# Kernel optimization log

Hardware: AMD Instinct MI355X
Metric: run time of the kernel (lower is better)

## Reference

```python
import jax, jax.numpy as jnp
import numpy as np

C = 64          # channels
HEADS = 4       # num_heads -> head_dim = 16
HID = int(C * 2.66)  # 170, GDFN hidden channels
B, H, W = 2, 256, 256


def conv1x1(x, w):
    # x: (b,c,h,w), w: (o,c) -> pointwise conv, no bias
    return jnp.einsum('bchw,oc->bohw', x, w)


def dwconv3x3(x, w):
    # depthwise 3x3, SAME padding; w: (C,1,3,3)
    return jax.lax.conv_general_dilated(
        x, w, window_strides=(1, 1), padding='SAME',
        feature_group_count=x.shape[1],
        dimension_numbers=('NCHW', 'OIHW', 'NCHW'))


def layer_norm_c(x, w, b):
    # torch: LayerNorm over channel dim of (b, hw, c), eps=1e-5
    mu = x.mean(axis=1, keepdims=True)
    var = ((x - mu) ** 2).mean(axis=1, keepdims=True)
    xn = (x - mu) / jnp.sqrt(var + 1e-5)
    return xn * w[None, :, None, None] + b[None, :, None, None]


def l2norm(x):
    # F.normalize(dim=-1), eps=1e-12
    n = jnp.sqrt(jnp.sum(x * x, axis=-1, keepdims=True))
    return x / jnp.maximum(n, 1e-12)


def mdta(x, temp, w_qkv, w_qkv_dw, w_po, w_kv, w_kv_dw, w_pof):
    b, c, h, w_ = x.shape
    d = c // HEADS
    qkv = dwconv3x3(conv1x1(x, w_qkv), w_qkv_dw)
    q, k, v = jnp.split(qkv, 3, axis=1)
    rs = lambda t: t.reshape(b, HEADS, d, h * w_)
    q, k, v = l2norm(rs(q)), l2norm(rs(k)), rs(v)
    # channel attention: (b,heads,d,d), softmax over last dim
    attn = jax.nn.softmax(jnp.einsum('bhdn,bhen->bhde', q, k) * temp, axis=-1)
    out = conv1x1(jnp.einsum('bhde,bhen->bhdn', attn, v).reshape(b, c, h, w_), w_po)
    # second gated branch: kv from `out`, reuse attn (qf/kf/attnf are dead code in source)
    kvf = dwconv3x3(conv1x1(out, w_kv), w_kv_dw)
    _kf, vf = jnp.split(kvf, 2, axis=1)
    vf = rs(vf)
    outf = conv1x1(jnp.einsum('bhde,bhen->bhdn', attn, vf).reshape(b, c, h, w_), w_pof)
    return outf


def gdfn(x, w_in, w_dw, w_out):
    x12 = dwconv3x3(conv1x1(x, w_in), w_dw)
    x1, x2 = jnp.split(x12, 2, axis=1)
    return conv1x1(jax.nn.gelu(x1, approximate=False) * x2, w_out)


def setup_inputs() -> dict:
    key = jax.random.key(0)
    ks = jax.random.split(key, 10)
    s = 0.05
    return {
        'x': jax.random.normal(ks[0], (B, C, H, W), jnp.float32),
        'n1_w': jnp.ones((C,), jnp.float32),
        'n1_b': jnp.zeros((C,), jnp.float32),
        'temp': jnp.ones((1, HEADS, 1, 1), jnp.float32),
        'w_qkv': jax.random.normal(ks[1], (3 * C, C), jnp.float32) * s,
        'w_qkv_dw': jax.random.normal(ks[2], (3 * C, 1, 3, 3), jnp.float32) * s,
        'w_po': jax.random.normal(ks[3], (C, C), jnp.float32) * s,
        'w_kv': jax.random.normal(ks[4], (2 * C, C), jnp.float32) * s,
        'w_kv_dw': jax.random.normal(ks[5], (2 * C, 1, 3, 3), jnp.float32) * s,
        'w_pof': jax.random.normal(ks[6], (C, C), jnp.float32) * s,
        'n2_w': jnp.ones((C,), jnp.float32),
        'n2_b': jnp.zeros((C,), jnp.float32),
        'w_in': jax.random.normal(ks[7], (2 * HID, C), jnp.float32) * s,
        'w_dw': jax.random.normal(ks[8], (2 * HID, 1, 3, 3), jnp.float32) * s,
        'w_out': jax.random.normal(ks[9], (C, HID), jnp.float32) * s,
    }


def reference(x, n1_w, n1_b, temp, w_qkv, w_qkv_dw, w_po, w_kv, w_kv_dw, w_pof,
              n2_w, n2_b, w_in, w_dw, w_out):
    x = x + mdta(layer_norm_c(x, n1_w, n1_b), temp,
                 w_qkv, w_qkv_dw, w_po, w_kv, w_kv_dw, w_pof)
    x = x + gdfn(layer_norm_c(x, n2_w, n2_b), w_in, w_dw, w_out)
    return x
```

## Files before the change

kernel.cpp:

```cpp
#include <hip/hip_runtime.h>
#include <hip/hip_bf16.h>
#include <math.h>

#define NPB 65536
#define BATCH 2
#define NTOT (BATCH * NPB)

typedef unsigned short u16;
typedef __attribute__((ext_vector_type(8))) short short8;
typedef __attribute__((ext_vector_type(4))) short short4v;
typedef __attribute__((ext_vector_type(4))) float f32x4;


__device__ __forceinline__ float bf2f(u16 u) {
  union { unsigned u; float f; } v; v.u = ((unsigned)u) << 16; return v.f;
}
__device__ __forceinline__ u16 f2bf(float f) {
  union { float f; unsigned u; } v; v.f = f;
  unsigned r = v.u + 0x7FFFu + ((v.u >> 16) & 1u);
  return (u16)(r >> 16);
}
__device__ __forceinline__ unsigned pk2(float a, float b) {
  return (unsigned)f2bf(a) | ((unsigned)f2bf(b) << 16);
}
__device__ __forceinline__ f32x4 mm(short8 a, short8 b, f32x4 c) {
  return __builtin_amdgcn_mfma_f32_16x16x32_bf16(a, b, c, 0, 0, 0);
}
__device__ __forceinline__ short8 ldfrag(const u16* F, int frag, int l) {
  return *reinterpret_cast<const short8*>(F + ((size_t)frag * 64 + l) * 8);
}
__device__ __forceinline__ void st4(u16* p, f32x4 c) {
  uint2 v; v.x = pk2(c[0], c[1]); v.y = pk2(c[2], c[3]);
  *reinterpret_cast<uint2*>(p) = v;
}
__device__ __forceinline__ float gelu_t(float a) {
  const float z = 0.7978845608f * fmaf(0.044715f * a, a * a, a);
  const float e = __expf(2.f * z);
  const float th = 1.f - 2.f / (e + 1.f);
  return 0.5f * a * (1.f + th);
}

__global__ __launch_bounds__(64) void k_wprep(
    const float* __restrict__ wqkv, const float* __restrict__ win,
    const float* __restrict__ wout, u16* __restrict__ WQf,
    u16* __restrict__ WIf, u16* __restrict__ WOf)
{
  const int f = blockIdx.x;
  const int l = threadIdx.x;
  const int fr = l & 15, fq = l >> 4;
  short8 v;
  u16* dst;
  if (f < 24) {
    const int t = f >> 1, kh = f & 1;
    const int row = t * 16 + fr;
#pragma unroll
    for (int j = 0; j < 8; ++j)
      v[j] = (short)f2bf(wqkv[(size_t)row * 64 + kh * 32 + fq * 8 + j]);
    dst = WQf + ((size_t)f * 64 + l) * 8;
  } else if (f < 68) {
    const int fi = f - 24;
    const int g = fi >> 1, kh = fi & 1;
    const int half = g / 11, t = g % 11;
    const int col = half * 176 + t * 16 + fr;
    const int row = col < 170 ? col : (col < 176 ? -1 : (col < 346 ? col - 6 : -1));
#pragma unroll
    for (int j = 0; j < 8; ++j)
      v[j] = (row < 0) ? (short)0
             : (short)f2bf(win[(size_t)row * 64 + kh * 32 + fq * 8 + j]);
    dst = WIf + ((size_t)fi * 64 + l) * 8;
  } else {
    const int fi = f - 68;
    const int t = fi / 6, kh = fi % 6;
    const int row = t * 16 + fr;
#pragma unroll
    for (int j = 0; j < 8; ++j) {
      const int k = kh * 32 + fq * 8 + j;
      v[j] = (k < 170) ? (short)f2bf(wout[(size_t)row * 170 + k]) : (short)0;
    }
    dst = WOf + ((size_t)fi * 64 + l) * 8;
  }
  *reinterpret_cast<short8*>(dst) = v;
}

__global__ __launch_bounds__(256, 4) void k_ln1(
    const float* __restrict__ x, const float* __restrict__ n1w,
    const float* __restrict__ n1b, u16* __restrict__ Y1)
{
  const int n = blockIdx.x * 256 + threadIdx.x;
  const int b = blockIdx.y;
  const size_t pix = (size_t)b * NPB + n;
  const float* xb = x + ((size_t)b * 64) * NPB + n;
  float y[64];
  float mu = 0.f;
#pragma unroll
  for (int c = 0; c < 64; ++c) { y[c] = xb[(size_t)c * NPB]; mu += y[c]; }
  mu *= (1.f / 64.f);
  float var = 0.f;
#pragma unroll
  for (int c = 0; c < 64; ++c) { float d = y[c] - mu; var = fmaf(d, d, var); }
  const float rstd = rsqrtf(var * (1.f / 64.f) + 1e-5f);
#pragma unroll
  for (int c = 0; c < 64; ++c) y[c] = (y[c] - mu) * rstd * n1w[c] + n1b[c];
#pragma unroll
  for (int cb = 0; cb < 4; ++cb) {
    u16* dst = Y1 + ((size_t)cb * NTOT + pix) * 16;
    uint4 v0, v1;
    v0.x = pk2(y[cb*16+0],  y[cb*16+1]);  v0.y = pk2(y[cb*16+2],  y[cb*16+3]);
    v0.z = pk2(y[cb*16+4],  y[cb*16+5]);  v0.w = pk2(y[cb*16+6],  y[cb*16+7]);
    v1.x = pk2(y[cb*16+8],  y[cb*16+9]);  v1.y = pk2(y[cb*16+10], y[cb*16+11]);
    v1.z = pk2(y[cb*16+12], y[cb*16+13]); v1.w = pk2(y[cb*16+14], y[cb*16+15]);
    *reinterpret_cast<uint4*>(dst) = v0;
    *reinterpret_cast<uint4*>(dst + 8) = v1;
  }
}

__global__ __launch_bounds__(256, 2) void g_qkvp(
    const u16* __restrict__ Y1, const u16* __restrict__ WQf,
    u16* __restrict__ qkvp)
{
  const int l = threadIdx.x & 63, fr = l & 15, fq = l >> 4;
  const int wv = blockIdx.x * 4 + (threadIdx.x >> 6);
  const int nw = gridDim.x * 4;
  short8 A[12][2];
#pragma unroll
  for (int t = 0; t < 12; ++t)
#pragma unroll
    for (int kh = 0; kh < 2; ++kh) A[t][kh] = ldfrag(WQf, t * 2 + kh, l);
  const size_t hof = (size_t)(fq & 1) * 8;
  for (int tile = wv; tile < 8192; tile += nw) {
    const size_t n = (size_t)tile * 16 + fr;
    const short8 b0 = *reinterpret_cast<const short8*>(
        Y1 + (((size_t)(fq >> 1)) * NTOT + n) * 16 + hof);
    const short8 b1 = *reinterpret_cast<const short8*>(
        Y1 + (((size_t)(2 + (fq >> 1))) * NTOT + n) * 16 + hof);
    f32x4 c[12];
#pragma unroll
    for (int t = 0; t < 12; ++t) c[t] = f32x4{0.f, 0.f, 0.f, 0.f};
#pragma unroll
    for (int t = 0; t < 12; ++t) c[t] = mm(A[t][0], b0, c[t]);
#pragma unroll
    for (int t = 0; t < 12; ++t) c[t] = mm(A[t][1], b1, c[t]);
#pragma unroll
    for (int t = 0; t < 12; ++t)
      st4(qkvp + ((size_t)t * NTOT + n) * 16 + fq * 4, c[t]);
  }
}

template<int STRIP>
__global__ __launch_bounds__(256, 4) void k_dwr4(
    const u16* __restrict__ in, u16* __restrict__ out,
    const float* __restrict__ wdw, int wofs)
{
  const int t = threadIdx.x;
  const int sub = t & 3, xi = t >> 2;
  const int q = blockIdx.x >> 2, xc = blockIdx.x & 3;
  const int strip = blockIdx.y, b = blockIdx.z;
  const int x = xc * 64 + xi;
  const int y0 = strip * STRIP;
  const int e0 = sub * 4;
  const u16* pin = in + ((size_t)q * NTOT + (size_t)b * NPB) * 16 + e0;

  float w[9][4];
#pragma unroll
  for (int ch = 0; ch < 4; ++ch) {
    const int row = wofs + q * 16 + e0 + ch;
#pragma unroll
    for (int tap = 0; tap < 9; ++tap) w[tap][ch] = wdw[(size_t)row * 9 + tap];
  }
  if (x == 0) {
#pragma unroll
    for (int ky = 0; ky < 3; ++ky)
#pragma unroll
      for (int ch = 0; ch < 4; ++ch) w[ky * 3 + 0][ch] = 0.f;
  }
  if (x == 255) {
#pragma unroll
    for (int ky = 0; ky < 3; ++ky)
#pragma unroll
      for (int ch = 0; ch < 4; ++ch) w[ky * 3 + 2][ch] = 0.f;
  }
  const int xl = x > 0 ? x - 1 : x;
  const int xr = x < 255 ? x + 1 : x;
  const size_t oL = (size_t)xl * 16, oC = (size_t)x * 16, oR = (size_t)xr * 16;

  short4v r[3][3];
  auto LDROW = [&](int yy, short4v* d) {
    if ((unsigned)yy < 256u) {
      const u16* rp = pin + (size_t)yy * 4096;
      d[0] = *reinterpret_cast<const short4v*>(rp + oL);
      d[1] = *reinterpret_cast<const short4v*>(rp + oC);
      d[2] = *reinterpret_cast<const short4v*>(rp + oR);
    } else {
      short4v z; z[0] = z[1] = z[2] = z[3] = 0;
      d[0] = z; d[1] = z; d[2] = z;
    }
  };
  LDROW(y0 - 1, r[0]);
  LDROW(y0, r[1]);
#pragma unroll 4
  for (int yy = 0; yy < STRIP; ++yy) {
    const int y = y0 + yy;
    LDROW(y + 1, r[2]);
    float acc[4] = {0.f, 0.f, 0.f, 0.f};
#pragma unroll
    for (int ky = 0; ky < 3; ++ky)
#pragma unroll
      for (int kx = 0; kx < 3; ++kx)
#pragma unroll
        for (int ch = 0; ch < 4; ++ch)
          acc[ch] = fmaf(w[ky * 3 + kx][ch], bf2f((u16)r[ky][kx][ch]), acc[ch]);
    uint2 o; o.x = pk2(acc[0], acc[1]); o.y = pk2(acc[2], acc[3]);
    *reinterpret_cast<uint2*>(
        out + ((size_t)q * NTOT + (size_t)b * NPB + (size_t)(y * 256 + x)) * 16 + e0) = o;
#pragma unroll
    for (int j = 0; j < 3; ++j) { r[0][j] = r[1][j]; r[1][j] = r[2][j]; }
  }
}

template<int STRIP>
__global__ __launch_bounds__(256, 4) void k_dwg(
    const u16* __restrict__ in, u16* __restrict__ out,
    const float* __restrict__ wdw)
{
  const int t = threadIdx.x;
  const int sub = t & 7, xi = t >> 3;
  const int pl = sub >> 2, cs = sub & 3;
  const int q = blockIdx.x >> 3, xc = blockIdx.x & 7;
  const int strip = blockIdx.y, b = blockIdx.z;
  const int x = xc * 32 + xi;
  const int y0 = strip * STRIP;
  const int e0 = cs * 4;
  const u16* pin = in + ((size_t)(q + pl * 11) * NTOT + (size_t)b * NPB) * 16 + e0;

  float w[9][4];
#pragma unroll
  for (int ch = 0; ch < 4; ++ch) {
    const int c = q * 16 + e0 + ch;
    const int row = pl * 170 + c;
    const bool valid = c < 170;
#pragma unroll
    for (int tap = 0; tap < 9; ++tap)
      w[tap][ch] = valid ? wdw[(size_t)row * 9 + tap] : 0.f;
  }
  if (x == 0) {
#pragma unroll
    for (int ky = 0; ky < 3; ++ky)
#pragma unroll
      for (int ch = 0; ch < 4; ++ch) w[ky * 3 + 0][ch] = 0.f;
  }
  if (x == 255) {
#pragma unroll
    for (int ky = 0; ky < 3; ++ky)
#pragma unroll
      for (int ch = 0; ch < 4; ++ch) w[ky * 3 + 2][ch] = 0.f;
  }
  const int xl = x > 0 ? x - 1 : x;
  const int xr = x < 255 ? x + 1 : x;
  const size_t oL = (size_t)xl * 16, oC = (size_t)x * 16, oR = (size_t)xr * 16;

  short4v r[3][3];
  auto LDROW = [&](int yy, short4v* d) {
    if ((unsigned)yy < 256u) {
      const u16* rp = pin + (size_t)yy * 4096;
      d[0] = *reinterpret_cast<const short4v*>(rp + oL);
      d[1] = *reinterpret_cast<const short4v*>(rp + oC);
      d[2] = *reinterpret_cast<const short4v*>(rp + oR);
    } else {
      short4v z; z[0] = z[1] = z[2] = z[3] = 0;
      d[0] = z; d[1] = z; d[2] = z;
    }
  };
  LDROW(y0 - 1, r[0]);
  LDROW(y0, r[1]);
#pragma unroll 4
  for (int yy = 0; yy < STRIP; ++yy) {
    const int y = y0 + yy;
    LDROW(y + 1, r[2]);
    float acc[4] = {0.f, 0.f, 0.f, 0.f};
#pragma unroll
    for (int ky = 0; ky < 3; ++ky)
#pragma unroll
      for (int kx = 0; kx < 3; ++kx)
#pragma unroll
        for (int ch = 0; ch < 4; ++ch)
          acc[ch] = fmaf(w[ky * 3 + kx][ch], bf2f((u16)r[ky][kx][ch]), acc[ch]);
    float o0 = __shfl_xor(acc[0], 4), o1 = __shfl_xor(acc[1], 4);
    float o2 = __shfl_xor(acc[2], 4), o3 = __shfl_xor(acc[3], 4);
    if (pl == 0) {
      float v[4];
      v[0] = gelu_t(acc[0]) * o0; v[1] = gelu_t(acc[1]) * o1;
      v[2] = gelu_t(acc[2]) * o2; v[3] = gelu_t(acc[3]) * o3;
      uint2 o; o.x = pk2(v[0], v[1]); o.y = pk2(v[2], v[3]);
      *reinterpret_cast<uint2*>(
          out + ((size_t)q * NTOT + (size_t)b * NPB + (size_t)(y * 256 + x)) * 16 + e0) = o;
    }
#pragma unroll
    for (int j = 0; j < 3; ++j) { r[0][j] = r[1][j]; r[1][j] = r[2][j]; }
  }
}

__global__ __launch_bounds__(256, 2) void k_gram_p(
    const u16* __restrict__ qkv, float* __restrict__ part)
{
  __shared__ __align__(16) u16 lds[32][520];
  const int chunk = blockIdx.x, h = blockIdx.y, b = blockIdx.z;
  const int t = threadIdx.x;
#pragma unroll
  for (int i = 0; i < 2; ++i) {
    const int p = t + i * 256;
    const size_t pix = (size_t)b * NPB + chunk * 512 + p;
    const u16* srcq = qkv + ((size_t)h * NTOT + pix) * 16;
    const u16* srck = qkv + ((size_t)(4 + h) * NTOT + pix) * 16;
    const short8 q0 = *reinterpret_cast<const short8*>(srcq);
    const short8 q1 = *reinterpret_cast<const short8*>(srcq + 8);
    const short8 k0 = *reinterpret_cast<const short8*>(srck);
    const short8 k1 = *reinterpret_cast<const short8*>(srck + 8);
#pragma unroll
    for (int j = 0; j < 8; ++j) {
      lds[j][p] = (u16)q0[j];  lds[8 + j][p] = (u16)q1[j];
      lds[16 + j][p] = (u16)k0[j]; lds[24 + j][p] = (u16)k1[j];
    }
  }
  __syncthreads();
  const int w = t >> 6, l = t & 63, fr = l & 15, fq = l >> 4;
  if (w >= 3) return;
  float* pp = part + ((size_t)((b * 4 + h) * 128) + chunk) * 288;
  const int rowA = (w == 2) ? 16 + fr : fr;
  const int rowB = (w == 0) ? 16 + fr : rowA;
  f32x4 acc = {0.f, 0.f, 0.f, 0.f};
#pragma unroll
  for (int kt = 0; kt < 16; ++kt) {
    const short8 a  = *reinterpret_cast<const short8*>(&lds[rowA][kt * 32 + fq * 8]);
    const short8 bb = *reinterpret_cast<const short8*>(&lds[rowB][kt * 32 + fq * 8]);
    acc = mm(a, bb, acc);
  }
  if (w == 0) {
#pragma unroll
    for (int r = 0; r < 4; ++r) pp[(fq * 4 + r) * 16 + fr] = acc[r];
  } else if ((fr >> 2) == fq) {
    pp[(w == 1 ? 256 : 272) + fr] = acc[fr & 3];
  }
}

__global__ __launch_bounds__(320) void k_gram_red(
    const float* __restrict__ part, float* __restrict__ G,
    float* __restrict__ Sq, float* __restrict__ Sk)
{
  const int bh = blockIdx.x;
  const int t = threadIdx.x;
  if (t >= 288) return;
  const float* p = part + (size_t)bh * 128 * 288 + t;
  float s = 0.f;
  for (int ch = 0; ch < 128; ++ch) s += p[(size_t)ch * 288];
  const int b = bh >> 2, h = bh & 3;
  if (t < 256) G[bh * 256 + t] = s;
  else if (t < 272) Sq[b * 64 + h * 16 + (t - 256)] = s;
  else Sk[b * 64 + h * 16 + (t - 272)] = s;
}

__global__ __launch_bounds__(256) void k_attn(
    const float* __restrict__ G, const float* __restrict__ Sq,
    const float* __restrict__ Sk, const float* __restrict__ temp,
    const float* __restrict__ wpo, const float* __restrict__ wkv,
    const float* __restrict__ wpof, u16* __restrict__ Pf,
    u16* __restrict__ M2f)
{
  __shared__ float attn[BATCH][4][16][16];
  __shared__ float M1[BATCH][64][64];
  __shared__ float rq[128], rk[128];
  const int t = threadIdx.x;
  if (t < 128) {
    rq[t] = 1.f / fmaxf(sqrtf(Sq[t]), 1e-12f);
    rk[t] = 1.f / fmaxf(sqrtf(Sk[t]), 1e-12f);
  }
  __syncthreads();
  if (t < 128) {
    const int b = t >> 6, h = (t >> 4) & 3, d = t & 15;
    const float tm = temp[h];
    const float* g = G + ((b * 4 + h) * 16 + d) * 16;
    const float rqd = rq[b * 64 + h * 16 + d];
    float L[16], mx = -1e30f;
#pragma unroll
    for (int e = 0; e < 16; ++e) {
      L[e] = g[e] * rqd * rk[b * 64 + h * 16 + e] * tm;
      mx = fmaxf(mx, L[e]);
    }
    float s = 0.f;
#pragma unroll
    for (int e = 0; e < 16; ++e) { L[e] = expf(L[e] - mx); s += L[e]; }
    const float inv = 1.f / s;
#pragma unroll
    for (int e = 0; e < 16; ++e) attn[b][h][d][e] = L[e] * inv;
  }
  __syncthreads();
  for (int s0 = 0; s0 < 32; ++s0) {
    const int idx = t * 32 + s0;
    const int b = idx >> 12, o = (idx >> 6) & 63, c = idx & 63;
    const int h = c >> 4, e = c & 15;
    float a = 0.f;
#pragma unroll
    for (int d = 0; d < 16; ++d) a = fmaf(wpo[o * 64 + h * 16 + d], attn[b][h][d][e], a);
    M1[b][o][c] = a;
  }
  __syncthreads();
  for (int it = 0; it < 4; ++it) {
    const int idx = it * 256 + t;
    const int l = idx & 63;
    const int fi = idx >> 6;
    const int b = fi >> 3, tt = (fi >> 1) & 3, kh = fi & 1;
    const int fr = l & 15, fq = l >> 4;
    const int o = tt * 16 + fr;
    short8 pv, mv;
#pragma unroll
    for (int j = 0; j < 8; ++j) {
      const int c = kh * 32 + fq * 8 + j;
      const int h = c >> 4, e = c & 15;
      float a2 = 0.f;
#pragma unroll
      for (int d = 0; d < 16; ++d)
        a2 = fmaf(wpof[o * 64 + h * 16 + d], attn[b][h][d][e], a2);
      mv[j] = (short)f2bf(a2);
      float a = 0.f;
      for (int jj = 0; jj < 64; ++jj)
        a = fmaf(wkv[(64 + o) * 64 + jj], M1[b][jj][c], a);
      pv[j] = (short)f2bf(a);
    }
    *reinterpret_cast<short8*>(Pf + ((size_t)fi * 64 + l) * 8) = pv;
    *reinterpret_cast<short8*>(M2f + ((size_t)fi * 64 + l) * 8) = mv;
  }
}

__global__ __launch_bounds__(256, 2) void g_pv(
    const u16* __restrict__ qkv, const u16* __restrict__ Pf,
    u16* __restrict__ vfp)
{
  const int l = threadIdx.x & 63, fr = l & 15, fq = l >> 4;
  const int wv = blockIdx.x * 4 + (threadIdx.x >> 6);
  const int nw = gridDim.x * 4;
  const int b = blockIdx.z;
  short8 A[4][2];
#pragma unroll
  for (int t = 0; t < 4; ++t)
#pragma unroll
    for (int kh = 0; kh < 2; ++kh)
      A[t][kh] = ldfrag(Pf, (b * 4 + t) * 2 + kh, l);
  const size_t hof = (size_t)(fq & 1) * 8;
  for (int tile = wv; tile < 4096; tile += nw) {
    const size_t n = (size_t)b * NPB + (size_t)tile * 16 + fr;
    const short8 b0 = *reinterpret_cast<const short8*>(
        qkv + ((size_t)(8 + (fq >> 1)) * NTOT + n) * 16 + hof);
    const short8 b1 = *reinterpret_cast<const short8*>(
        qkv + ((size_t)(10 + (fq >> 1)) * NTOT + n) * 16 + hof);
    f32x4 c[4];
#pragma unroll
    for (int t = 0; t < 4; ++t) c[t] = f32x4{0.f, 0.f, 0.f, 0.f};
#pragma unroll
    for (int t = 0; t < 4; ++t) c[t] = mm(A[t][0], b0, c[t]);
#pragma unroll
    for (int t = 0; t < 4; ++t) c[t] = mm(A[t][1], b1, c[t]);
#pragma unroll
    for (int t = 0; t < 4; ++t)
      st4(vfp + ((size_t)t * NTOT + n) * 16 + fq * 4, c[t]);
  }
}

__global__ __launch_bounds__(256, 2) void g_x2ln(
    const u16* __restrict__ vf, const u16* __restrict__ M2f,
    const float* __restrict__ x, const float* __restrict__ n2w,
    const float* __restrict__ n2b, u16* __restrict__ X2,
    u16* __restrict__ Y2)
{
  const int l = threadIdx.x & 63, fr = l & 15, fq = l >> 4;
  const int wv = blockIdx.x * 4 + (threadIdx.x >> 6);
  const int nw = gridDim.x * 4;
  const int b = blockIdx.z;
  short8 A[4][2];
#pragma unroll
  for (int t = 0; t < 4; ++t)
#pragma unroll
    for (int kh = 0; kh < 2; ++kh)
      A[t][kh] = ldfrag(M2f, (b * 4 + t) * 2 + kh, l);
  const size_t hof = (size_t)(fq & 1) * 8;
  for (int tile = wv; tile < 4096; tile += nw) {
    const int pix0 = tile * 16;
    const size_t n = (size_t)b * NPB + pix0 + fr;
    const short8 b0 = *reinterpret_cast<const short8*>(
        vf + ((size_t)(fq >> 1) * NTOT + n) * 16 + hof);
    const short8 b1 = *reinterpret_cast<const short8*>(
        vf + ((size_t)(2 + (fq >> 1)) * NTOT + n) * 16 + hof);
    f32x4 c[4];
#pragma unroll
    for (int t = 0; t < 4; ++t) c[t] = f32x4{0.f, 0.f, 0.f, 0.f};
#pragma unroll
    for (int t = 0; t < 4; ++t) c[t] = mm(A[t][0], b0, c[t]);
#pragma unroll
    for (int t = 0; t < 4; ++t) c[t] = mm(A[t][1], b1, c[t]);
    const int pix = pix0 + fr;
#pragma unroll
    for (int t = 0; t < 4; ++t)
#pragma unroll
      for (int r = 0; r < 4; ++r)
        c[t][r] += x[((size_t)(b * 64 + t * 16 + fq * 4 + r)) * NPB + pix];
#pragma unroll
    for (int t = 0; t < 4; ++t)
      st4(X2 + ((size_t)t * NTOT + n) * 16 + fq * 4, c[t]);
    float s = 0.f;
#pragma unroll
    for (int t = 0; t < 4; ++t)
#pragma unroll
      for (int r = 0; r < 4; ++r) s += c[t][r];
    s += __shfl_xor(s, 16); s += __shfl_xor(s, 32);
    const float mu = s * (1.f / 64.f);
    float ss = 0.f;
#pragma unroll
    for (int t = 0; t < 4; ++t)
#pragma unroll
      for (int r = 0; r < 4; ++r) { float d = c[t][r] - mu; ss = fmaf(d, d, ss); }
    ss += __shfl_xor(ss, 16); ss += __shfl_xor(ss, 32);
    const float rstd = rsqrtf(ss * (1.f / 64.f) + 1e-5f);
#pragma unroll
    for (int t = 0; t < 4; ++t)
#pragma unroll
      for (int r = 0; r < 4; ++r) {
        const int oc = t * 16 + fq * 4 + r;
        c[t][r] = (c[t][r] - mu) * rstd * n2w[oc] + n2b[oc];
      }
#pragma unroll
    for (int t = 0; t < 4; ++t)
      st4(Y2 + ((size_t)t * NTOT + n) * 16 + fq * 4, c[t]);
  }
}

__global__ __launch_bounds__(256, 2) void g_win(
    const u16* __restrict__ Y2, const u16* __restrict__ WIf,
    u16* __restrict__ hpre)
{
  const int l = threadIdx.x & 63, fr = l & 15, fq = l >> 4;
  const int wv = blockIdx.x * 4 + (threadIdx.x >> 6);
  const int nw = gridDim.x * 4;
  const int half = wv & 1;
  short8 A[11][2];
#pragma unroll
  for (int t = 0; t < 11; ++t)
#pragma unroll
    for (int kh = 0; kh < 2; ++kh)
      A[t][kh] = ldfrag(WIf, (half * 11 + t) * 2 + kh, l);
  const size_t hof = (size_t)(fq & 1) * 8;
  for (int tile = wv >> 1; tile < 8192; tile += (nw >> 1)) {
    const size_t n = (size_t)tile * 16 + fr;
    const short8 b0 = *reinterpret_cast<const short8*>(
        Y2 + ((size_t)(fq >> 1) * NTOT + n) * 16 + hof);
    const short8 b1 = *reinterpret_cast<const short8*>(
        Y2 + ((size_t)(2 + (fq >> 1)) * NTOT + n) * 16 + hof);
    f32x4 c[11];
#pragma unroll
    for (int t = 0; t < 11; ++t) c[t] = f32x4{0.f, 0.f, 0.f, 0.f};
#pragma unroll
    for (int t = 0; t < 11; ++t) c[t] = mm(A[t][0], b0, c[t]);
#pragma unroll
    for (int t = 0; t < 11; ++t) c[t] = mm(A[t][1], b1, c[t]);
#pragma unroll
    for (int t = 0; t < 11; ++t)
      st4(hpre + ((size_t)(half * 11 + t) * NTOT + n) * 16 + fq * 4, c[t]);
  }
}

__global__ __launch_bounds__(256, 2) void g_out(
    const u16* __restrict__ hg, const u16* __restrict__ WOf,
    const u16* __restrict__ X2, float* __restrict__ out)
{
  const int l = threadIdx.x & 63, fr = l & 15, fq = l >> 4;
  const int wv = blockIdx.x * 4 + (threadIdx.x >> 6);
  const int nw = gridDim.x * 4;
  short8 A[4][6];
#pragma unroll
  for (int t = 0; t < 4; ++t)
#pragma unroll
    for (int kh = 0; kh < 6; ++kh)
      A[t][kh] = ldfrag(WOf, t * 6 + kh, l);
  const size_t hof = (size_t)(fq & 1) * 8;
  for (int tile = wv; tile < 8192; tile += nw) {
    const size_t n = (size_t)tile * 16 + fr;
    short8 bb[6];
#pragma unroll
    for (int kh = 0; kh < 6; ++kh) {
      int hb = kh * 2 + (fq >> 1);
      if (hb > 10) hb = 10;
      bb[kh] = *reinterpret_cast<const short8*>(
          hg + ((size_t)hb * NTOT + n) * 16 + hof);
    }
    f32x4 c[4];
#pragma unroll
    for (int t = 0; t < 4; ++t) c[t] = f32x4{0.f, 0.f, 0.f, 0.f};
#pragma unroll
    for (int kh = 0; kh < 6; ++kh)
#pragma unroll
      for (int t = 0; t < 4; ++t) c[t] = mm(A[t][kh], bb[kh], c[t]);
    const int b = (int)(n >> 16);
    const int pix = (int)(n & 65535);
#pragma unroll
    for (int t = 0; t < 4; ++t) {
      const uint2 xv = *reinterpret_cast<const uint2*>(
          X2 + ((size_t)t * NTOT + n) * 16 + fq * 4);
      const u16 h0 = (u16)(xv.x & 0xffff), h1 = (u16)(xv.x >> 16);
      const u16 h2 = (u16)(xv.y & 0xffff), h3 = (u16)(xv.y >> 16);
      const int ocb = b * 64 + t * 16 + fq * 4;
      out[((size_t)(ocb + 0)) * NPB + pix] = c[t][0] + bf2f(h0);
      out[((size_t)(ocb + 1)) * NPB + pix] = c[t][1] + bf2f(h1);
      out[((size_t)(ocb + 2)) * NPB + pix] = c[t][2] + bf2f(h2);
      out[((size_t)(ocb + 3)) * NPB + pix] = c[t][3] + bf2f(h3);
    }
  }
}

extern "C" void kernel_launch(void* const* d_in, const int* in_sizes, int n_in,
                              void* d_out, int out_size, void* d_ws, size_t ws_size,
                              hipStream_t stream)
{
  const float* x     = (const float*)d_in[0];
  const float* n1w   = (const float*)d_in[1];
  const float* n1b   = (const float*)d_in[2];
  const float* temp  = (const float*)d_in[3];
  const float* wqkv  = (const float*)d_in[4];
  const float* wqkvd = (const float*)d_in[5];
  const float* wpo   = (const float*)d_in[6];
  const float* wkv   = (const float*)d_in[7];
  const float* wkvd  = (const float*)d_in[8];
  const float* wpof  = (const float*)d_in[9];
  const float* n2w   = (const float*)d_in[10];
  const float* n2b   = (const float*)d_in[11];
  const float* win   = (const float*)d_in[12];
  const float* wdw   = (const float*)d_in[13];
  const float* wout  = (const float*)d_in[14];
  float* out = (float*)d_out;

  char* ws = (char*)d_ws;
  const size_t offA  = 0;
  const size_t offB  = 16777216;
  const size_t offC  = offB + 50331648;
  const size_t offHg = offC + 50331648;
  const size_t offX2 = offHg + 46137344 + 256;
  const size_t offSm = offX2 + 16777216;

  u16* Y1   = (u16*)(ws + offA);
  u16* VFP  = (u16*)(ws + offA);
  u16* Y2   = (u16*)(ws + offA);
  u16* QKVp = (u16*)(ws + offB);
  u16* VF   = (u16*)(ws + offB);
  u16* Hpre = (u16*)(ws + offB);
  u16* QKV  = (u16*)(ws + offC);
  u16* Hg   = (u16*)(ws + offHg);
  u16* X2   = (u16*)(ws + offX2);
  float* part = (float*)(ws + offSm);
  float* G    = (float*)(ws + offSm + 1179648);
  float* Sq   = (float*)(ws + offSm + 1179648 + 8192);
  float* Sk   = (float*)(ws + offSm + 1179648 + 8704);
  u16* Pf     = (u16*)(ws + offSm + 1179648 + 9216);
  u16* M2f    = (u16*)(ws + offSm + 1179648 + 25600);
  u16* WQf    = (u16*)(ws + offSm + 1179648 + 41984);
  u16* WIf    = (u16*)(ws + offSm + 1179648 + 66560);
  u16* WOf    = (u16*)(ws + offSm + 1179648 + 111616);

  k_wprep<<<dim3(92), 64, 0, stream>>>(wqkv, win, wout, WQf, WIf, WOf);
  k_ln1<<<dim3(NPB / 256, BATCH), 256, 0, stream>>>(x, n1w, n1b, Y1);
  g_qkvp<<<dim3(512), 256, 0, stream>>>(Y1, WQf, QKVp);
  k_dwr4<16><<<dim3(48, 16, BATCH), 256, 0, stream>>>(QKVp, QKV, wqkvd, 0);
  k_gram_p<<<dim3(128, 4, BATCH), 256, 0, stream>>>(QKV, part);
  k_gram_red<<<dim3(BATCH * 4), 320, 0, stream>>>(part, G, Sq, Sk);
  k_attn<<<dim3(1), 256, 0, stream>>>(G, Sq, Sk, temp, wpo, wkv, wpof, Pf, M2f);
  g_pv<<<dim3(256, 1, BATCH), 256, 0, stream>>>(QKV, Pf, VFP);
  k_dwr4<8><<<dim3(16, 32, BATCH), 256, 0, stream>>>(VFP, VF, wkvd, 64);
  g_x2ln<<<dim3(256, 1, BATCH), 256, 0, stream>>>(VF, M2f, x, n2w, n2b, X2, Y2);
  g_win<<<dim3(512), 256, 0, stream>>>(Y2, WIf, Hpre);
  k_dwg<16><<<dim3(88, 16, BATCH), 256, 0, stream>>>(Hpre, Hg, wdw);
  g_out<<<dim3(512), 256, 0, stream>>>(Hg, WOf, X2, out);
}
```

Before: 254.6 us.

## Rework depthwise convs with float row ring and per-thread gate pairing

The depthwise 3x3 kernels now convert each loaded bf16 row to float once and keep it in a three-slot register ring with a fully unrolled strip loop. This replaces reconverting the same values three times and copying rows between registers. The gated kernel k_dwg now has each thread load and convolve both the GELU half and the gate half, removing the cross-lane shuffle and the idle half of the lanes. That halves its grid and lowers launch bounds to 2 because of the extra registers. The GEMM-style kernels also get doubled grid sizes, which is only safe if they use grid-stride loops; the larger register footprint may also cut occupancy.

New measurement: 268.2 us. +5.3%, slower.

```diff
diff --git a/kernel.cpp b/kernel.cpp
--- a/kernel.cpp
+++ b/kernel.cpp
@@ -167,135 +167,161 @@
 #pragma unroll
     for (int tap = 0; tap < 9; ++tap) w[tap][ch] = wdw[(size_t)row * 9 + tap];
   }
-  if (x == 0) {
+  if (x == 0)
 #pragma unroll
     for (int ky = 0; ky < 3; ++ky)
 #pragma unroll
       for (int ch = 0; ch < 4; ++ch) w[ky * 3 + 0][ch] = 0.f;
-  }
-  if (x == 255) {
+  if (x == 255)
 #pragma unroll
     for (int ky = 0; ky < 3; ++ky)
 #pragma unroll
       for (int ch = 0; ch < 4; ++ch) w[ky * 3 + 2][ch] = 0.f;
-  }
   const int xl = x > 0 ? x - 1 : x;
   const int xr = x < 255 ? x + 1 : x;
   const size_t oL = (size_t)xl * 16, oC = (size_t)x * 16, oR = (size_t)xr * 16;
 
-  short4v r[3][3];
-  auto LDROW = [&](int yy, short4v* d) {
+  float wn[3][3][4];
+  auto LDF = [&](int yy, int slot) {
     if ((unsigned)yy < 256u) {
       const u16* rp = pin + (size_t)yy * 4096;
-      d[0] = *reinterpret_cast<const short4v*>(rp + oL);
-      d[1] = *reinterpret_cast<const short4v*>(rp + oC);
-      d[2] = *reinterpret_cast<const short4v*>(rp + oR);
+      const short4v a0 = *reinterpret_cast<const short4v*>(rp + oL);
+      const short4v a1 = *reinterpret_cast<const short4v*>(rp + oC);
+      const short4v a2 = *reinterpret_cast<const short4v*>(rp + oR);
+#pragma unroll
+      for (int ch = 0; ch < 4; ++ch) {
+        wn[slot][0][ch] = bf2f((u16)a0[ch]);
+        wn[slot][1][ch] = bf2f((u16)a1[ch]);
+        wn[slot][2][ch] = bf2f((u16)a2[ch]);
+      }
     } else {
-      short4v z; z[0] = z[1] = z[2] = z[3] = 0;
-      d[0] = z; d[1] = z; d[2] = z;
+#pragma unroll
+      for (int dx = 0; dx < 3; ++dx)
+#pragma unroll
+        for (int ch = 0; ch < 4; ++ch) wn[slot][dx][ch] = 0.f;
     }
   };
-  LDROW(y0 - 1, r[0]);
-  LDROW(y0, r[1]);
-#pragma unroll 4
+  LDF(y0 - 1, 0);
+  LDF(y0, 1);
+#pragma unroll
   for (int yy = 0; yy < STRIP; ++yy) {
-    const int y = y0 + yy;
-    LDROW(y + 1, r[2]);
+    const int s0 = yy % 3, s1 = (yy + 1) % 3, s2 = (yy + 2) % 3;
+    LDF(y0 + yy + 1, s2);
     float acc[4] = {0.f, 0.f, 0.f, 0.f};
 #pragma unroll
-    for (int ky = 0; ky < 3; ++ky)
-#pragma unroll
-      for (int kx = 0; kx < 3; ++kx)
-#pragma unroll
-        for (int ch = 0; ch < 4; ++ch)
-          acc[ch] = fmaf(w[ky * 3 + kx][ch], bf2f((u16)r[ky][kx][ch]), acc[ch]);
+    for (int kx = 0; kx < 3; ++kx)
+#pragma unroll
+      for (int ch = 0; ch < 4; ++ch) {
+        acc[ch] = fmaf(w[0 * 3 + kx][ch], wn[s0][kx][ch], acc[ch]);
+        acc[ch] = fmaf(w[1 * 3 + kx][ch], wn[s1][kx][ch], acc[ch]);
+        acc[ch] = fmaf(w[2 * 3 + kx][ch], wn[s2][kx][ch], acc[ch]);
+      }
     uint2 o; o.x = pk2(acc[0], acc[1]); o.y = pk2(acc[2], acc[3]);
     *reinterpret_cast<uint2*>(
-        out + ((size_t)q * NTOT + (size_t)b * NPB + (size_t)(y * 256 + x)) * 16 + e0) = o;
-#pragma unroll
-    for (int j = 0; j < 3; ++j) { r[0][j] = r[1][j]; r[1][j] = r[2][j]; }
+        out + ((size_t)q * NTOT + (size_t)b * NPB +
+               (size_t)((y0 + yy) * 256 + x)) * 16 + e0) = o;
   }
 }
 
 template<int STRIP>
-__global__ __launch_bounds__(256, 4) void k_dwg(
+__global__ __launch_bounds__(256, 2) void k_dwg(
     const u16* __restrict__ in, u16* __restrict__ out,
     const float* __restrict__ wdw)
 {
   const int t = threadIdx.x;
-  const int sub = t & 7, xi = t >> 3;
-  const int pl = sub >> 2, cs = sub & 3;
-  const int q = blockIdx.x >> 3, xc = blockIdx.x & 7;
+  const int sub = t & 3, xi = t >> 2;
+  const int q = blockIdx.x >> 2, xc = blockIdx.x & 3;
   const int strip = blockIdx.y, b = blockIdx.z;
-  const int x = xc * 32 + xi;
+  const int x = xc * 64 + xi;
   const int y0 = strip * STRIP;
-  const int e0 = cs * 4;
-  const u16* pin = in + ((size_t)(q + pl * 11) * NTOT + (size_t)b * NPB) * 16 + e0;
-
-  float w[9][4];
-#pragma unroll
-  for (int ch = 0; ch < 4; ++ch) {
-    const int c = q * 16 + e0 + ch;
-    const int row = pl * 170 + c;
-    const bool valid = c < 170;
-#pragma unroll
-    for (int tap = 0; tap < 9; ++tap)
-      w[tap][ch] = valid ? wdw[(size_t)row * 9 + tap] : 0.f;
-  }
-  if (x == 0) {
-#pragma unroll
-    for (int ky = 0; ky < 3; ++ky)
-#pragma unroll
-      for (int ch = 0; ch < 4; ++ch) w[ky * 3 + 0][ch] = 0.f;
-  }
-  if (x == 255) {
-#pragma unroll
-    for (int ky = 0; ky < 3; ++ky)
-#pragma unroll
-      for (int ch = 0; ch < 4; ++ch) w[ky * 3 + 2][ch] = 0.f;
-  }
+  const int e0 = sub * 4;
+  const u16* pin0 = in + ((size_t)q * NTOT + (size_t)b * NPB) * 16 + e0;
+  const u16* pin1 = in + ((size_t)(11 + q) * NTOT + (size_t)b * NPB) * 16 + e0;
+
+  float w[2][9][4];
+#pragma unroll
+  for (int pl = 0; pl < 2; ++pl)
+#pragma unroll
+    for (int ch = 0; ch < 4; ++ch) {
+      const int c = q * 16 + e0 + ch;
+      const bool valid = c < 170;
+      const int row = pl * 170 + c;
+#pragma unroll
+      for (int tap = 0; tap < 9; ++tap)
+        w[pl][tap][ch] = valid ? wdw[(size_t)row * 9 + tap] : 0.f;
+    }
+  if (x == 0)
+#pragma unroll
+    for (int pl = 0; pl < 2; ++pl)
+#pragma unroll
+      for (int ky = 0; ky < 3; ++ky)
+#pragma unroll
+        for (int ch = 0; ch < 4; ++ch) w[pl][ky * 3 + 0][ch] = 0.f;
+  if (x == 255)
+#pragma unroll
+    for (int pl = 0; pl < 2; ++pl)
+#pragma unroll
+      for (int ky = 0; ky < 3; ++ky)
+#pragma unroll
+        for (int ch = 0; ch < 4; ++ch) w[pl][ky * 3 + 2][ch] = 0.f;
   const int xl = x > 0 ? x - 1 : x;
   const int xr = x < 255 ? x + 1 : x;
   const size_t oL = (size_t)xl * 16, oC = (size_t)x * 16, oR = (size_t)xr * 16;
 
-  short4v r[3][3];
-  auto LDROW = [&](int yy, short4v* d) {
+  float wn[3][2][3][4];
+  auto LDF = [&](int yy, int slot) {
     if ((unsigned)yy < 256u) {
-      const u16* rp = pin + (size_t)yy * 4096;
-      d[0] = *reinterpret_cast<const short4v*>(rp + oL);
-      d[1] = *reinterpret_cast<const short4v*>(rp + oC);
-      d[2] = *reinterpret_cast<const short4v*>(rp + oR);
+      const u16* rp0 = pin0 + (size_t)yy * 4096;
+      const u16* rp1 = pin1 + (size_t)yy * 4096;
+      const short4v a0 = *reinterpret_cast<const short4v*>(rp0 + oL);
+      const short4v a1 = *reinterpret_cast<const short4v*>(rp0 + oC);
+      const short4v a2 = *reinterpret_cast<const short4v*>(rp0 + oR);
+      const short4v g0 = *reinterpret_cast<const short4v*>(rp1 + oL);
+      const short4v g1 = *reinterpret_cast<const short4v*>(rp1 + oC);
+      const short4v g2 = *reinterpret_cast<const short4v*>(rp1 + oR);
+#pragma unroll
+      for (int ch = 0; ch < 4; ++ch) {
+        wn[slot][0][0][ch] = bf2f((u16)a0[ch]);
+        wn[slot][0][1][ch] = bf2f((u16)a1[ch]);
+        wn[slot][0][2][ch] = bf2f((u16)a2[ch]);
+        wn[slot][1][0][ch] = bf2f((u16)g0[ch]);
+        wn[slot][1][1][ch] = bf2f((u16)g1[ch]);
+        wn[slot][1][2][ch] = bf2f((u16)g2[ch]);
+      }
     } else {
-      short4v z; z[0] = z[1] = z[2] = z[3] = 0;
-      d[0] = z; d[1] = z; d[2] = z;
+#pragma unroll
+      for (int pl = 0; pl < 2; ++pl)
+#pragma unroll
+        for (int dx = 0; dx < 3; ++dx)
+#pragma unroll
+          for (int ch = 0; ch < 4; ++ch) wn[slot][pl][dx][ch] = 0.f;
     }
   };
-  LDROW(y0 - 1, r[0]);
-  LDROW(y0, r[1]);
-#pragma unroll 4
+  LDF(y0 - 1, 0);
+  LDF(y0, 1);
+#pragma unroll
   for (int yy = 0; yy < STRIP; ++yy) {
-    const int y = y0 + yy;
-    LDROW(y + 1, r[2]);
-    float acc[4] = {0.f, 0.f, 0.f, 0.f};
-#pragma unroll
-    for (int ky = 0; ky < 3; ++ky)
+    const int s0 = yy % 3, s1 = (yy + 1) % 3, s2 = (yy + 2) % 3;
+    LDF(y0 + yy + 1, s2);
+    float acc[2][4] = {{0.f, 0.f, 0.f, 0.f}, {0.f, 0.f, 0.f, 0.f}};
+#pragma unroll
+    for (int pl = 0; pl < 2; ++pl)
 #pragma unroll
       for (int kx = 0; kx < 3; ++kx)
 #pragma unroll
-        for (int ch = 0; ch < 4; ++ch)
-          acc[ch] = fmaf(w[ky * 3 + kx][ch], bf2f((u16)r[ky][kx][ch]), acc[ch]);
-    float o0 = __shfl_xor(acc[0], 4), o1 = __shfl_xor(acc[1], 4);
-    float o2 = __shfl_xor(acc[2], 4), o3 = __shfl_xor(acc[3], 4);
-    if (pl == 0) {
-      float v[4];
-      v[0] = gelu_t(acc[0]) * o0; v[1] = gelu_t(acc[1]) * o1;
-      v[2] = gelu_t(acc[2]) * o2; v[3] = gelu_t(acc[3]) * o3;
-      uint2 o; o.x = pk2(v[0], v[1]); o.y = pk2(v[2], v[3]);
-      *reinterpret_cast<uint2*>(
-          out + ((size_t)q * NTOT + (size_t)b * NPB + (size_t)(y * 256 + x)) * 16 + e0) = o;
-    }
-#pragma unroll
-    for (int j = 0; j < 3; ++j) { r[0][j] = r[1][j]; r[1][j] = r[2][j]; }
+        for (int ch = 0; ch < 4; ++ch) {
+          acc[pl][ch] = fmaf(w[pl][0 * 3 + kx][ch], wn[s0][pl][kx][ch], acc[pl][ch]);
+          acc[pl][ch] = fmaf(w[pl][1 * 3 + kx][ch], wn[s1][pl][kx][ch], acc[pl][ch]);
+          acc[pl][ch] = fmaf(w[pl][2 * 3 + kx][ch], wn[s2][pl][kx][ch], acc[pl][ch]);
+        }
+    float v[4];
+#pragma unroll
+    for (int ch = 0; ch < 4; ++ch)
+      v[ch] = gelu_t(acc[0][ch]) * acc[1][ch];
+    uint2 o; o.x = pk2(v[0], v[1]); o.y = pk2(v[2], v[3]);
+    *reinterpret_cast<uint2*>(
+        out + ((size_t)q * NTOT + (size_t)b * NPB +
+               (size_t)((y0 + yy) * 256 + x)) * 16 + e0) = o;
   }
 }
 
@@ -663,15 +689,15 @@
 
   k_wprep<<<dim3(92), 64, 0, stream>>>(wqkv, win, wout, WQf, WIf, WOf);
   k_ln1<<<dim3(NPB / 256, BATCH), 256, 0, stream>>>(x, n1w, n1b, Y1);
-  g_qkvp<<<dim3(512), 256, 0, stream>>>(Y1, WQf, QKVp);
+  g_qkvp<<<dim3(1024), 256, 0, stream>>>(Y1, WQf, QKVp);
   k_dwr4<16><<<dim3(48, 16, BATCH), 256, 0, stream>>>(QKVp, QKV, wqkvd, 0);
   k_gram_p<<<dim3(128, 4, BATCH), 256, 0, stream>>>(QKV, part);
   k_gram_red<<<dim3(BATCH * 4), 320, 0, stream>>>(part, G, Sq, Sk);
   k_attn<<<dim3(1), 256, 0, stream>>>(G, Sq, Sk, temp, wpo, wkv, wpof, Pf, M2f);
-  g_pv<<<dim3(256, 1, BATCH), 256, 0, stream>>>(QKV, Pf, VFP);
+  g_pv<<<dim3(512, 1, BATCH), 256, 0, stream>>>(QKV, Pf, VFP);
   k_dwr4<8><<<dim3(16, 32, BATCH), 256, 0, stream>>>(VFP, VF, wkvd, 64);
-  g_x2ln<<<dim3(256, 1, BATCH), 256, 0, stream>>>(VF, M2f, x, n2w, n2b, X2, Y2);
-  g_win<<<dim3(512), 256, 0, stream>>>(Y2, WIf, Hpre);
-  k_dwg<16><<<dim3(88, 16, BATCH), 256, 0, stream>>>(Hpre, Hg, wdw);
-  g_out<<<dim3(512), 256, 0, stream>>>(Hg, WOf, X2, out);
-}
+  g_x2ln<<<dim3(512, 1, BATCH), 256, 0, stream>>>(VF, M2f, x, n2w, n2b, X2, Y2);
+  g_win<<<dim3(1024), 256, 0, stream>>>(Y2, WIf, Hpre);
+  k_dwg<16><<<dim3(44, 16, BATCH), 256, 0, stream>>>(Hpre, Hg, wdw);
+  g_out<<<dim3(1024), 256, 0, stream>>>(Hg, WOf, X2, out);
+}
```
